# Kernel tuning notes

Measured on AMD Instinct MI355X. Metric: run time of the kernel, lower is better.

## Reference

```python
import jax, jax.numpy as jnp
import numpy as np

D = 768   # embedding_len
NL = 4    # nleft attributes
NR = 4    # nright attributes
LL = 256  # total left tokens
LR = 256  # total right tokens
DE = (NL + NR) * D  # entity-matching highway width


def setup_inputs() -> dict:
    key = jax.random.key(0)
    ks = jax.random.split(key, 12)
    f = lambda k, s: (jax.random.normal(k, s, jnp.float32) * 0.02)
    return {
        "left_emb": jax.random.normal(ks[0], (LL, D), jnp.float32),
        "right_emb": jax.random.normal(ks[1], (LR, D), jnp.float32),
        "Wn_tok": f(ks[2], (D, D)), "bn_tok": jnp.zeros((D,), jnp.float32),
        "Wg_tok": f(ks[3], (D, D)), "bg_tok": jnp.full((D,), -2.0, jnp.float32),
        "W_lin_tok": f(ks[4], (D, 1)), "b_lin_tok": jnp.zeros((1,), jnp.float32),
        "attr_emb_left": f(ks[5], (NL, D)),
        "attr_emb_right": f(ks[6], (NR, D)),
        "Wn_ent": f(ks[7], (DE, DE)), "bn_ent": jnp.zeros((DE,), jnp.float32),
        "Wg_ent": f(ks[8], (DE, DE)), "bg_ent": jnp.full((DE,), -2.0, jnp.float32),
        "W_lin_ent": f(ks[9], (DE, 2)), "b_lin_ent": jnp.zeros((2,), jnp.float32),
        "empty_attr_res": f(ks[10], (D,)),
        # per-attribute token counts; left includes an empty attribute
        "left_attrs_len": jnp.array([100, 80, 76, 0], dtype=jnp.int32),
        "right_attrs_len": jnp.array([64, 64, 64, 64], dtype=jnp.int32),
    }


def _highway(x, Wn, bn, Wg, bg):
    h = jax.nn.relu(x @ Wn + bn)
    g = jax.nn.sigmoid(x @ Wg + bg)
    return h * g + (1.0 - g) * x


def _token_matching(left, right, Wn, bn, Wg, bg, W_lin, b_lin):
    # compare_matrix: [L_left, L_right, D]
    cmp = jnp.abs(left[:, None, :] - right[None, :, :])
    hw = _highway(cmp, Wn, bn, Wg, bg)
    scores = hw @ W_lin + b_lin                     # [Ll, Lr, 1]
    # softmax over dim=1 (right tokens); only argmax is used downstream
    idx = jnp.argmax(scores[..., 0], axis=1)        # [Ll]
    return jnp.take_along_axis(cmp, idx[:, None, None], axis=1)[:, 0, :]  # [Ll, D]


def _attribute_matching(tokens, field_emb, cmp_res, lens, empty_attr):
    # ragged per-attribute softmax-weighted segment reduction
    n = field_emb.shape[0]
    L = tokens.shape[0]
    seg = jnp.repeat(jnp.arange(n), lens, total_repeat_length=L)   # [L]
    scores = jnp.einsum('ld,ld->l', tokens, field_emb[seg])        # [L]
    m = jax.ops.segment_max(scores, seg, num_segments=n)
    e = jnp.exp(scores - m[seg])
    z = jax.ops.segment_sum(e, seg, num_segments=n)
    w = e / z[seg]                                                  # softmax within segment
    reps = jax.ops.segment_sum(w[:, None] * cmp_res, seg, num_segments=n)  # [n, D]
    return jnp.where(lens[:, None] > 0, reps, empty_attr[None, :])


def reference(left_emb, right_emb, Wn_tok, bn_tok, Wg_tok, bg_tok,
              W_lin_tok, b_lin_tok, attr_emb_left, attr_emb_right,
              Wn_ent, bn_ent, Wg_ent, bg_ent, W_lin_ent, b_lin_ent,
              empty_attr_res, left_attrs_len, right_attrs_len):
    left_cmp = _token_matching(left_emb, right_emb, Wn_tok, bn_tok, Wg_tok, bg_tok,
                               W_lin_tok, b_lin_tok)
    right_cmp = _token_matching(right_emb, left_emb, Wn_tok, bn_tok, Wg_tok, bg_tok,
                                W_lin_tok, b_lin_tok)
    left_rep = _attribute_matching(left_emb, attr_emb_left, left_cmp,
                                   left_attrs_len, empty_attr_res)
    right_rep = _attribute_matching(right_emb, attr_emb_right, right_cmp,
                                    right_attrs_len, empty_attr_res)
    concat = jnp.concatenate([left_rep, right_rep], axis=0).reshape(1, -1)  # [1, DE]
    hw = _highway(concat, Wn_ent, bn_ent, Wg_ent, bg_ent)
    logits = hw @ W_lin_ent + b_lin_ent                                     # [1, 2]
    return jax.nn.softmax(logits, axis=1).flatten()                         # [2]
```

## Files before the change

### kernel.cpp

```cpp
#include <hip/hip_runtime.h>
#include <math.h>
#include <stdint.h>

#define DD 768
#define NT 256
#define DE 6144

typedef _Float16 half8 __attribute__((ext_vector_type(8)));
typedef _Float16 half4 __attribute__((ext_vector_type(4)));
typedef short short8 __attribute__((ext_vector_type(8)));
typedef float floatx4 __attribute__((ext_vector_type(4)));

__device__ __forceinline__ void async_ld16(const void* g, void* l) {
  __builtin_amdgcn_global_load_lds(
      (const __attribute__((address_space(1))) unsigned int*)g,
      (__attribute__((address_space(3))) unsigned int*)l, 16, 0, 0);
}

__global__ __launch_bounds__(256) void transpose_cvt(
    const float* __restrict__ Wn, const float* __restrict__ Wg,
    _Float16* __restrict__ WnT, _Float16* __restrict__ WgT)
{
  const float* W = blockIdx.z ? Wg : Wn;
  _Float16* WT = blockIdx.z ? WgT : WnT;
  __shared__ float tile[32][33];
  const int tx = threadIdx.x & 31, ty = threadIdx.x >> 5;
  const int d0 = blockIdx.x * 32, k0 = blockIdx.y * 32;
  #pragma unroll
  for (int p = 0; p < 4; ++p)
    tile[ty + p*8][tx] = W[(size_t)(k0 + ty + p*8)*DD + d0 + tx];
  __syncthreads();
  #pragma unroll
  for (int p = 0; p < 4; ++p) {
    const int d = d0 + ty + p*8;
    const int k = k0 + tx;
    const int idx = d*DD + (k & ~63) + ((((k >> 3) & 7) ^ (d & 7)) << 3) + (k & 7);
    WT[idx] = (_Float16)tile[tx][ty + p*8];
  }
}

__global__ __launch_bounds__(256) void cvt_lr(
    const float* __restrict__ L, const float* __restrict__ R,
    _Float16* __restrict__ Lh, _Float16* __restrict__ Rh)
{
  const float* src = blockIdx.y ? R : L;
  _Float16* dst = blockIdx.y ? Rh : Lh;
  const int o = blockIdx.x*1024 + threadIdx.x*4;
  float4 v = *(const float4*)&src[o];
  half4 h; h[0] = (_Float16)v.x; h[1] = (_Float16)v.y;
  h[2] = (_Float16)v.z; h[3] = (_Float16)v.w;
  *(half4*)&dst[o] = h;
}

__global__ __launch_bounds__(256, 2) void score_mfma(
    const _Float16* __restrict__ Lh, const _Float16* __restrict__ Rh,
    const _Float16* __restrict__ WnT, const _Float16* __restrict__ WgT,
    const float* __restrict__ bn, const float* __restrict__ bg,
    const float* __restrict__ Wl, float* __restrict__ Sp)
{
  const int jbase = blockIdx.x * 128;
  const int dbase = blockIdx.y * 128;
  const int i     = blockIdx.z;
  const int tid   = threadIdx.x;

  __shared__ _Float16 As [128*64];
  __shared__ _Float16 Bns[128*64];
  __shared__ _Float16 Bgs[128*64];

  floatx4 accn[4][4] = {};
  floatx4 accg[4][4] = {};

  const int kg = tid & 7;
  const int rl = tid >> 3;

  const int lane = tid & 63;
  const int wid  = tid >> 6;
  const int wj = (wid & 1) * 64;
  const int wd = (wid >> 1) * 64;
  const int m = lane & 15;
  const int q = lane >> 4;
  const int gq8 = ((q ^ (m & 7)) << 3);

  const int drow = lane >> 3;
  const int dseg = lane & 7;

  int aoff[4], boff[4];
  #pragma unroll
  for (int t4 = 0; t4 < 4; ++t4) {
    aoff[t4] = (wj + t4*16 + m) * 64;
    boff[t4] = (wd + t4*16 + m) * 64;
  }

  for (int k0 = 0; k0 < DD; k0 += 64) {
    #pragma unroll
    for (int t = 0; t < 4; ++t) {
      const int row = wid*32 + t*8 + drow;
      async_ld16(&WnT[(size_t)(dbase + row)*DD + k0 + dseg*8],
                 &Bns[(wid*32 + t*8)*64]);
      async_ld16(&WgT[(size_t)(dbase + row)*DD + k0 + dseg*8],
                 &Bgs[(wid*32 + t*8)*64]);
    }
    half8 l8 = *(const half8*)&Lh[i*DD + k0 + kg*8];
    #pragma unroll
    for (int rep = 0; rep < 4; ++rep) {
      const int row = rl + rep*32;
      half8 rv = *(const half8*)&Rh[(size_t)(jbase + row)*DD + k0 + kg*8];
      half8 dv8 = l8 - rv;
      short8 sb; __builtin_memcpy(&sb, &dv8, 16);
      sb &= (short)0x7FFF;
      *(short8*)&As[row*64 + ((kg ^ (row & 7)) << 3)] = sb;
    }
    __syncthreads();
    #pragma unroll
    for (int kk = 0; kk < 64; kk += 32) {
      const int ko = kk ^ gq8;
      half8 af[4], bfn[4], bfg[4];
      #pragma unroll
      for (int t4 = 0; t4 < 4; ++t4) af[t4] = *(const half8*)&As[aoff[t4] + ko];
      #pragma unroll
      for (int t4 = 0; t4 < 4; ++t4) {
        bfn[t4] = *(const half8*)&Bns[boff[t4] + ko];
        bfg[t4] = *(const half8*)&Bgs[boff[t4] + ko];
      }
      #pragma unroll
      for (int tj = 0; tj < 4; ++tj)
        #pragma unroll
        for (int td = 0; td < 4; ++td) {
          accn[tj][td] = __builtin_amdgcn_mfma_f32_16x16x32_f16(
              af[tj], bfn[td], accn[tj][td], 0, 0, 0);
          accg[tj][td] = __builtin_amdgcn_mfma_f32_16x16x32_f16(
              af[tj], bfg[td], accg[tj][td], 0, 0, 0);
        }
    }
    __syncthreads();
  }

  float bnv[4], bgv[4], wlv[4], lv[4];
  int dv[4];
  #pragma unroll
  for (int td = 0; td < 4; ++td) {
    const int d = dbase + wd + td*16 + m;
    dv[td] = d; bnv[td] = bn[d]; bgv[td] = bg[d]; wlv[td] = Wl[d];
    lv[td] = (float)Lh[i*DD + d];
  }
  const int jb = jbase + wj;
  const int plane = blockIdx.y * 2 + (wid >> 1);
  float* Sout = Sp + (size_t)plane * NT * NT + (size_t)i * NT;
  #pragma unroll
  for (int tj = 0; tj < 4; ++tj) {
    #pragma unroll
    for (int r = 0; r < 4; ++r) {
      const int j = jb + tj*16 + q*4 + r;
      float sc = 0.f;
      #pragma unroll
      for (int td = 0; td < 4; ++td) {
        const float nv = accn[tj][td][r] + bnv[td];
        const float gp = accg[tj][td][r] + bgv[td];
        const float g  = 1.f / (1.f + __expf(-gp));
        const float c  = fabsf(lv[td] - (float)Rh[(size_t)j*DD + dv[td]]);
        sc += (fmaxf(nv, 0.f)*g + (1.f - g)*c) * wlv[td];
      }
      sc += __shfl_xor(sc, 1, 16);
      sc += __shfl_xor(sc, 2, 16);
      sc += __shfl_xor(sc, 4, 16);
      sc += __shfl_xor(sc, 8, 16);
      if (m == 0) Sout[j] = sc;
    }
  }
}

__global__ __launch_bounds__(256) void argmax_attr(
    const float* __restrict__ Sp,
    int* __restrict__ idxL, int* __restrict__ idxR,
    const float* __restrict__ Lemb, const float* __restrict__ Remb,
    const float* __restrict__ AEl, const float* __restrict__ AEr,
    const int* __restrict__ lensL, const int* __restrict__ lensR,
    float* __restrict__ wS, int* __restrict__ segA)
{
  const int b = blockIdx.x;
  const int t = threadIdx.x;

  if (b < 2*NT) {
    const size_t off = (b < NT) ? ((size_t)b*NT + t) : ((size_t)t*NT + (b - NT));
    float v = 0.f;
    #pragma unroll
    for (int p = 0; p < 12; ++p) v += Sp[(size_t)p*NT*NT + off];
    int idx = t;
    #pragma unroll
    for (int mm = 1; mm < 64; mm <<= 1) {
      float ov = __shfl_xor(v, mm, 64);
      int   oi = __shfl_xor(idx, mm, 64);
      if (ov > v || (ov == v && oi < idx)) { v = ov; idx = oi; }
    }
    __shared__ float sv[4]; __shared__ int si[4];
    if ((t & 63) == 0) { sv[t>>6] = v; si[t>>6] = idx; }
    __syncthreads();
    if (t == 0) {
      #pragma unroll
      for (int w = 1; w < 4; ++w)
        if (sv[w] > v || (sv[w] == v && si[w] < idx)) { v = sv[w]; idx = si[w]; }
      if (b < NT) idxL[b] = idx; else idxR[b - NT] = idx;
    }
    return;
  }

  const int side = b - 2*NT;
  const float* tok = side ? Remb : Lemb;
  const float* AE  = side ? AEr  : AEl;
  const int* lens  = side ? lensR : lensL;
  const int c0 = lens[0], c1 = c0 + lens[1], c2 = c1 + lens[2];
  const int seg = (t < c0) ? 0 : (t < c1) ? 1 : (t < c2) ? 2 : 3;
  float s = 0.f;
  const float4* tr = (const float4*)&tok[(size_t)t*DD];
  const float4* ar = (const float4*)&AE[(size_t)seg*DD];
  for (int k = 0; k < DD/4; ++k) {
    float4 a = tr[k], bb = ar[k];
    s += a.x*bb.x + a.y*bb.y + a.z*bb.z + a.w*bb.w;
  }
  __shared__ float scS[NT]; __shared__ int segS[NT];
  __shared__ float mS[4], zS[4];
  scS[t] = s; segS[t] = seg;
  __syncthreads();
  if (t < 4) {
    float mx = -INFINITY;
    for (int u = 0; u < NT; ++u) if (segS[u] == t) mx = fmaxf(mx, scS[u]);
    mS[t] = mx;
    float z = 0.f;
    for (int u = 0; u < NT; ++u) if (segS[u] == t) z += __expf(scS[u] - mx);
    zS[t] = z;
  }
  __syncthreads();
  wS[side*NT + t] = __expf(s - mS[seg]) / zS[seg];
  segA[side*NT + t] = seg;
}

__global__ __launch_bounds__(256) void attr_reduce(
    const float* __restrict__ Lemb, const float* __restrict__ Remb,
    const int* __restrict__ lensL, const int* __restrict__ lensR,
    const int* __restrict__ idxL, const int* __restrict__ idxR,
    const float* __restrict__ wS, const int* __restrict__ segA,
    const float* __restrict__ empty, float* __restrict__ x)
{
  const int side = blockIdx.x;
  const float* tok = side ? Remb : Lemb;
  const float* oth = side ? Lemb : Remb;
  const int* lens  = side ? lensR : lensL;
  const int* idx   = side ? idxR  : idxL;
  const float* w   = wS + side*NT;
  const int* sg    = segA + side*NT;
  float* xo = x + side*4*DD;
  const int t = threadIdx.x;
  const int dl = t & 63, uq = t >> 6;
  const int d = blockIdx.y*64 + dl;
  float a0 = 0.f, a1 = 0.f, a2 = 0.f, a3 = 0.f;
  for (int u = uq*64; u < uq*64 + 64; ++u) {
    const float c = fabsf(tok[(size_t)u*DD + d] - oth[(size_t)idx[u]*DD + d]);
    const float wc = w[u] * c;
    const int s = sg[u];
    a0 += (s == 0) ? wc : 0.f;
    a1 += (s == 1) ? wc : 0.f;
    a2 += (s == 2) ? wc : 0.f;
    a3 += (s == 3) ? wc : 0.f;
  }
  __shared__ float red[4][4][64];
  red[uq][0][dl] = a0; red[uq][1][dl] = a1;
  red[uq][2][dl] = a2; red[uq][3][dl] = a3;
  __syncthreads();
  if (uq == 0) {
    #pragma unroll
    for (int s = 0; s < 4; ++s) {
      float v = red[0][s][dl] + red[1][s][dl] + red[2][s][dl] + red[3][s][dl];
      xo[s*DD + d] = (lens[s] > 0) ? v : empty[d];
    }
  }
}

__global__ __launch_bounds__(256) void ent_matvec4(
    const float* __restrict__ x,
    const float* __restrict__ Wn, const float* __restrict__ Wg,
    float* __restrict__ pn, float* __restrict__ pg)
{
  const float* W = blockIdx.z ? Wg : Wn;
  float* p = blockIdx.z ? pg : pn;
  __shared__ float xs[96];
  const int db = blockIdx.x;
  const int kb = blockIdx.y;
  const int tid = threadIdx.x;
  if (tid < 96) xs[tid] = x[kb*96 + tid];
  __syncthreads();
  const int col = db*1024 + tid*4;
  float4 a = {0.f,0.f,0.f,0.f};
  const size_t base = (size_t)kb*96*DE + col;
  #pragma unroll 8
  for (int kk = 0; kk < 96; ++kk) {
    const float xv = xs[kk];
    float4 w = *(const float4*)&W[base + (size_t)kk*DE];
    a.x = fmaf(xv, w.x, a.x); a.y = fmaf(xv, w.y, a.y);
    a.z = fmaf(xv, w.z, a.z); a.w = fmaf(xv, w.w, a.w);
  }
  *(float4*)&p[(size_t)kb*DE + col] = a;
}

__global__ __launch_bounds__(256) void ent_reduce(
    const float* __restrict__ pn, const float* __restrict__ pg,
    float* __restrict__ yn, float* __restrict__ yg)
{
  const int o = blockIdx.x*256 + threadIdx.x;
  float sn = 0.f, sg = 0.f;
  for (int kb = 0; kb < 64; ++kb) {
    sn += pn[(size_t)kb*DE + o];
    sg += pg[(size_t)kb*DE + o];
  }
  yn[o] = sn; yg[o] = sg;
}

__global__ __launch_bounds__(256) void final_kernel(
    const float* __restrict__ x, const float* __restrict__ yn,
    const float* __restrict__ yg, const float* __restrict__ bn,
    const float* __restrict__ bg, const float* __restrict__ Wl,
    const float* __restrict__ bl, float* __restrict__ out)
{
  const int tid = threadIdx.x;
  float a0 = 0.f, a1 = 0.f;
  for (int p = 0; p < DE/256; ++p) {
    int d = p*256 + tid;
    float n  = yn[d] + bn[d];
    float gp = yg[d] + bg[d];
    float h  = fmaxf(n, 0.f);
    float g  = 1.f / (1.f + __expf(-gp));
    float hw = h*g + (1.f - g)*x[d];
    a0 += hw * Wl[d*2 + 0];
    a1 += hw * Wl[d*2 + 1];
  }
  #pragma unroll
  for (int mm = 1; mm < 64; mm <<= 1) {
    a0 += __shfl_xor(a0, mm, 64);
    a1 += __shfl_xor(a1, mm, 64);
  }
  __shared__ float s0[4], s1[4];
  if ((tid & 63) == 0) { s0[tid>>6] = a0; s1[tid>>6] = a1; }
  __syncthreads();
  if (tid == 0) {
    for (int w = 1; w < 4; ++w) { a0 += s0[w]; a1 += s1[w]; }
    float l0 = a0 + bl[0], l1 = a1 + bl[1];
    float m = fmaxf(l0, l1);
    float e0 = __expf(l0 - m), e1 = __expf(l1 - m);
    out[0] = e0 / (e0 + e1);
    out[1] = e1 / (e0 + e1);
  }
}

extern "C" void kernel_launch(void* const* d_in, const int* in_sizes, int n_in,
                              void* d_out, int out_size, void* d_ws, size_t ws_size,
                              hipStream_t stream) {
  const float* Lemb   = (const float*)d_in[0];
  const float* Remb   = (const float*)d_in[1];
  const float* Wn_tok = (const float*)d_in[2];
  const float* bn_tok = (const float*)d_in[3];
  const float* Wg_tok = (const float*)d_in[4];
  const float* bg_tok = (const float*)d_in[5];
  const float* Wl_tok = (const float*)d_in[6];
  const float* AEl    = (const float*)d_in[8];
  const float* AEr    = (const float*)d_in[9];
  const float* Wn_ent = (const float*)d_in[10];
  const float* bn_ent = (const float*)d_in[11];
  const float* Wg_ent = (const float*)d_in[12];
  const float* bg_ent = (const float*)d_in[13];
  const float* Wl_ent = (const float*)d_in[14];
  const float* bl_ent = (const float*)d_in[15];
  const float* empty  = (const float*)d_in[16];
  const int*   lensL  = (const int*)d_in[17];
  const int*   lensR  = (const int*)d_in[18];

  char* ws = (char*)d_ws;
  float* Sp   = (float*)(ws + 0);
  float* pn   = (float*)(ws + 0);
  float* pg   = (float*)(ws + 1572864);
  int*  idxL  = (int*)  (ws + 3145728);
  int*  idxR  = (int*)  (ws + 3146752);
  float* x    = (float*)(ws + 3147776);
  float* yn   = (float*)(ws + 3172352);
  float* yg   = (float*)(ws + 3196928);
  float* wSm  = (float*)(ws + 3221504);
  int*  segA  = (int*)  (ws + 3223552);
  _Float16* WnT = (_Float16*)(ws + 3225600);
  _Float16* WgT = (_Float16*)(ws + 4405248);
  _Float16* Lh  = (_Float16*)(ws + 5584896);
  _Float16* Rh  = (_Float16*)(ws + 5978112);

  transpose_cvt<<<dim3(24, 24, 2), 256, 0, stream>>>(Wn_tok, Wg_tok, WnT, WgT);
  cvt_lr<<<dim3(192, 2), 256, 0, stream>>>(Lemb, Remb, Lh, Rh);
  score_mfma<<<dim3(2, 6, NT), 256, 0, stream>>>(
      Lh, Rh, WnT, WgT, bn_tok, bg_tok, Wl_tok, Sp);
  argmax_attr<<<514, 256, 0, stream>>>(
      Sp, idxL, idxR, Lemb, Remb, AEl, AEr, lensL, lensR, wSm, segA);
  attr_reduce<<<dim3(2, 12), 256, 0, stream>>>(
      Lemb, Remb, lensL, lensR, idxL, idxR, wSm, segA, empty, x);
  ent_matvec4<<<dim3(6, 64, 2), 256, 0, stream>>>(x, Wn_ent, Wg_ent, pn, pg);
  ent_reduce<<<24, 256, 0, stream>>>(pn, pg, yn, yg);
  final_kernel<<<1, 256, 0, stream>>>(
      x, yn, yg, bn_ent, bg_ent, Wl_ent, bl_ent, (float*)d_out);
}
```

Before: 649.8 us.

## Double-buffer LDS tiles in score_mfma to overlap loads with MFMA

After: 768.8 us. 1.18x slower.

```diff
diff --git a/kernel.cpp b/kernel.cpp
--- a/kernel.cpp
+++ b/kernel.cpp
@@ -63,9 +63,9 @@
   const int i     = blockIdx.z;
   const int tid   = threadIdx.x;
 
-  __shared__ _Float16 As [128*64];
-  __shared__ _Float16 Bns[128*64];
-  __shared__ _Float16 Bgs[128*64];
+  __shared__ _Float16 As [2][128*64];
+  __shared__ _Float16 Bns[2][128*64];
+  __shared__ _Float16 Bgs[2][128*64];
 
   floatx4 accn[4][4] = {};
   floatx4 accg[4][4] = {};
@@ -91,14 +91,14 @@
     boff[t4] = (wd + t4*16 + m) * 64;
   }
 
-  for (int k0 = 0; k0 < DD; k0 += 64) {
+  auto stage = [&](int k0, _Float16* As_, _Float16* Bns_, _Float16* Bgs_) {
     #pragma unroll
     for (int t = 0; t < 4; ++t) {
       const int row = wid*32 + t*8 + drow;
       async_ld16(&WnT[(size_t)(dbase + row)*DD + k0 + dseg*8],
-                 &Bns[(wid*32 + t*8)*64]);
+                 &Bns_[(wid*32 + t*8)*64]);
       async_ld16(&WgT[(size_t)(dbase + row)*DD + k0 + dseg*8],
-                 &Bgs[(wid*32 + t*8)*64]);
+                 &Bgs_[(wid*32 + t*8)*64]);
     }
     half8 l8 = *(const half8*)&Lh[i*DD + k0 + kg*8];
     #pragma unroll
@@ -108,19 +108,22 @@
       half8 dv8 = l8 - rv;
       short8 sb; __builtin_memcpy(&sb, &dv8, 16);
       sb &= (short)0x7FFF;
-      *(short8*)&As[row*64 + ((kg ^ (row & 7)) << 3)] = sb;
-    }
-    __syncthreads();
+      *(short8*)&As_[row*64 + ((kg ^ (row & 7)) << 3)] = sb;
+    }
+  };
+
+  auto compute = [&](const _Float16* As_, const _Float16* Bns_,
+                     const _Float16* Bgs_) {
     #pragma unroll
     for (int kk = 0; kk < 64; kk += 32) {
       const int ko = kk ^ gq8;
       half8 af[4], bfn[4], bfg[4];
       #pragma unroll
-      for (int t4 = 0; t4 < 4; ++t4) af[t4] = *(const half8*)&As[aoff[t4] + ko];
+      for (int t4 = 0; t4 < 4; ++t4) af[t4] = *(const half8*)&As_[aoff[t4] + ko];
       #pragma unroll
       for (int t4 = 0; t4 < 4; ++t4) {
-        bfn[t4] = *(const half8*)&Bns[boff[t4] + ko];
-        bfg[t4] = *(const half8*)&Bgs[boff[t4] + ko];
+        bfn[t4] = *(const half8*)&Bns_[boff[t4] + ko];
+        bfg[t4] = *(const half8*)&Bgs_[boff[t4] + ko];
       }
       #pragma unroll
       for (int tj = 0; tj < 4; ++tj)
@@ -132,6 +135,17 @@
               af[tj], bfg[td], accg[tj][td], 0, 0, 0);
         }
     }
+  };
+
+  stage(0, As[0], Bns[0], Bgs[0]);
+  __syncthreads();
+
+  for (int t = 0; t < 12; t += 2) {
+    stage((t + 1)*64, As[1], Bns[1], Bgs[1]);
+    compute(As[0], Bns[0], Bgs[0]);
+    __syncthreads();
+    if (t + 2 < 12) stage((t + 2)*64, As[0], Bns[0], Bgs[0]);
+    compute(As[1], Bns[1], Bgs[1]);
     __syncthreads();
   }
 
```

## Double-buffer score_mfma LDS tiles and widen blocks to cover all right tokens

Applied to the files above, without the earlier changes.

Result: slower. 669.6 us (+3.1%).

```diff
diff --git a/kernel.cpp b/kernel.cpp
--- a/kernel.cpp
+++ b/kernel.cpp
@@ -52,20 +52,19 @@
   *(half4*)&dst[o] = h;
 }
 
-__global__ __launch_bounds__(256, 2) void score_mfma(
+__global__ __launch_bounds__(512, 2) void score_mfma(
     const _Float16* __restrict__ Lh, const _Float16* __restrict__ Rh,
     const _Float16* __restrict__ WnT, const _Float16* __restrict__ WgT,
     const float* __restrict__ bn, const float* __restrict__ bg,
     const float* __restrict__ Wl, float* __restrict__ Sp)
 {
-  const int jbase = blockIdx.x * 128;
-  const int dbase = blockIdx.y * 128;
-  const int i     = blockIdx.z;
+  const int dbase = blockIdx.x * 128;
+  const int i     = blockIdx.y;
   const int tid   = threadIdx.x;
 
-  __shared__ _Float16 As [128*64];
-  __shared__ _Float16 Bns[128*64];
-  __shared__ _Float16 Bgs[128*64];
+  __shared__ _Float16 As [2][256*64];
+  __shared__ _Float16 Bns[2][128*64];
+  __shared__ _Float16 Bgs[2][128*64];
 
   floatx4 accn[4][4] = {};
   floatx4 accg[4][4] = {};
@@ -75,8 +74,8 @@
 
   const int lane = tid & 63;
   const int wid  = tid >> 6;
-  const int wj = (wid & 1) * 64;
-  const int wd = (wid >> 1) * 64;
+  const int wj = (wid & 3) * 64;
+  const int wd = (wid >> 2) * 64;
   const int m = lane & 15;
   const int q = lane >> 4;
   const int gq8 = ((q ^ (m & 7)) << 3);
@@ -84,55 +83,102 @@
   const int drow = lane >> 3;
   const int dseg = lane & 7;
 
-  int aoff[4], boff[4];
+  int arow[4], brow[4];
   #pragma unroll
   for (int t4 = 0; t4 < 4; ++t4) {
-    aoff[t4] = (wj + t4*16 + m) * 64;
-    boff[t4] = (wd + t4*16 + m) * 64;
-  }
-
-  for (int k0 = 0; k0 < DD; k0 += 64) {
-    #pragma unroll
-    for (int t = 0; t < 4; ++t) {
-      const int row = wid*32 + t*8 + drow;
-      async_ld16(&WnT[(size_t)(dbase + row)*DD + k0 + dseg*8],
-                 &Bns[(wid*32 + t*8)*64]);
-      async_ld16(&WgT[(size_t)(dbase + row)*DD + k0 + dseg*8],
-                 &Bgs[(wid*32 + t*8)*64]);
-    }
-    half8 l8 = *(const half8*)&Lh[i*DD + k0 + kg*8];
+    arow[t4] = (wj + t4*16 + m) * 64;
+    brow[t4] = (wd + t4*16 + m) * 64;
+  }
+
+  {
+    half8 l80 = *(const half8*)&Lh[i*DD + kg*8];
+    #pragma unroll
+    for (int tt = 0; tt < 2; ++tt) {
+      const int brow0 = wid*16 + tt*8;
+      async_ld16(&WnT[(size_t)(dbase + brow0 + drow)*DD + dseg*8],
+                 &Bns[0][brow0*64]);
+      async_ld16(&WgT[(size_t)(dbase + brow0 + drow)*DD + dseg*8],
+                 &Bgs[0][brow0*64]);
+    }
     #pragma unroll
     for (int rep = 0; rep < 4; ++rep) {
-      const int row = rl + rep*32;
-      half8 rv = *(const half8*)&Rh[(size_t)(jbase + row)*DD + k0 + kg*8];
-      half8 dv8 = l8 - rv;
+      const int row = rl + rep*64;
+      half8 rv = *(const half8*)&Rh[(size_t)row*DD + kg*8];
+      half8 dv8 = l80 - rv;
       short8 sb; __builtin_memcpy(&sb, &dv8, 16);
       sb &= (short)0x7FFF;
-      *(short8*)&As[row*64 + ((kg ^ (row & 7)) << 3)] = sb;
+      *(short8*)&As[0][row*64 + ((kg ^ (row & 7)) << 3)] = sb;
     }
     __syncthreads();
-    #pragma unroll
-    for (int kk = 0; kk < 64; kk += 32) {
-      const int ko = kk ^ gq8;
-      half8 af[4], bfn[4], bfg[4];
+  }
+
+  for (int t = 0; t < 12; ++t) {
+    const int c = t & 1;
+    const _Float16* Ac  = As [c];
+    const _Float16* Bnc = Bns[c];
+    const _Float16* Bgc = Bgs[c];
+    _Float16* An  = As [c ^ 1];
+    _Float16* Bnn = Bns[c ^ 1];
+    _Float16* Bgn = Bgs[c ^ 1];
+    const int k0n = (t + 1) * 64;
+    const bool st = (t < 11);
+
+    half8 l8n;
+    if (st) l8n = *(const half8*)&Lh[i*DD + k0n + kg*8];
+
+    #pragma unroll
+    for (int p = 0; p < 4; ++p) {
+      const int jh = p >> 1, dh = p & 1;
+      half8 af[2][2], bfn[2][2], bfg[2][2];
       #pragma unroll
-      for (int t4 = 0; t4 < 4; ++t4) af[t4] = *(const half8*)&As[aoff[t4] + ko];
+      for (int kki = 0; kki < 2; ++kki) {
+        const int ko = (kki*32) ^ gq8;
+        #pragma unroll
+        for (int u = 0; u < 2; ++u) {
+          af [kki][u] = *(const half8*)&Ac [arow[jh*2 + u] + ko];
+          bfn[kki][u] = *(const half8*)&Bnc[brow[dh*2 + u] + ko];
+          bfg[kki][u] = *(const half8*)&Bgc[brow[dh*2 + u] + ko];
+        }
+      }
+      half8 rv;
+      if (st) {
+        rv = *(const half8*)&Rh[(size_t)(rl + p*64)*DD + k0n + kg*8];
+        const int tt = p & 1;
+        const int brow0 = wid*16 + tt*8;
+        if (p < 2) {
+          async_ld16(&WnT[(size_t)(dbase + brow0 + drow)*DD + k0n + dseg*8],
+                     &Bnn[brow0*64]);
+        } else {
+          async_ld16(&WgT[(size_t)(dbase + brow0 + drow)*DD + k0n + dseg*8],
+                     &Bgn[brow0*64]);
+        }
+      }
+      __builtin_amdgcn_sched_barrier(0);
+      __builtin_amdgcn_s_barrier();
+      __builtin_amdgcn_sched_barrier(0);
+      __builtin_amdgcn_s_setprio(1);
       #pragma unroll
-      for (int t4 = 0; t4 < 4; ++t4) {
-        bfn[t4] = *(const half8*)&Bns[boff[t4] + ko];
-        bfg[t4] = *(const half8*)&Bgs[boff[t4] + ko];
+      for (int kki = 0; kki < 2; ++kki)
+        #pragma unroll
+        for (int u = 0; u < 2; ++u)
+          #pragma unroll
+          for (int v = 0; v < 2; ++v) {
+            accn[jh*2+u][dh*2+v] = __builtin_amdgcn_mfma_f32_16x16x32_f16(
+                af[kki][u], bfn[kki][v], accn[jh*2+u][dh*2+v], 0, 0, 0);
+            accg[jh*2+u][dh*2+v] = __builtin_amdgcn_mfma_f32_16x16x32_f16(
+                af[kki][u], bfg[kki][v], accg[jh*2+u][dh*2+v], 0, 0, 0);
+          }
+      __builtin_amdgcn_s_setprio(0);
+      if (st) {
+        const int row = rl + p*64;
+        half8 dv8 = l8n - rv;
+        short8 sb; __builtin_memcpy(&sb, &dv8, 16);
+        sb &= (short)0x7FFF;
+        *(short8*)&An[row*64 + ((kg ^ (row & 7)) << 3)] = sb;
       }
-      #pragma unroll
-      for (int tj = 0; tj < 4; ++tj)
-        #pragma unroll
-        for (int td = 0; td < 4; ++td) {
-          accn[tj][td] = __builtin_amdgcn_mfma_f32_16x16x32_f16(
-              af[tj], bfn[td], accn[tj][td], 0, 0, 0);
-          accg[tj][td] = __builtin_amdgcn_mfma_f32_16x16x32_f16(
-              af[tj], bfg[td], accg[tj][td], 0, 0, 0);
-        }
-    }
-    __syncthreads();
+      __builtin_amdgcn_sched_barrier(0);
+      __syncthreads();
+    }
   }
 
   float bnv[4], bgv[4], wlv[4], lv[4];
@@ -143,8 +189,8 @@
     dv[td] = d; bnv[td] = bn[d]; bgv[td] = bg[d]; wlv[td] = Wl[d];
     lv[td] = (float)Lh[i*DD + d];
   }
-  const int jb = jbase + wj;
-  const int plane = blockIdx.y * 2 + (wid >> 1);
+  const int jb = wj;
+  const int plane = blockIdx.x * 2 + (wid >> 2);
   float* Sout = Sp + (size_t)plane * NT * NT + (size_t)i * NT;
   #pragma unroll
   for (int tj = 0; tj < 4; ++tj) {
@@ -390,7 +436,7 @@
 
   transpose_cvt<<<dim3(24, 24, 2), 256, 0, stream>>>(Wn_tok, Wg_tok, WnT, WgT);
   cvt_lr<<<dim3(192, 2), 256, 0, stream>>>(Lemb, Remb, Lh, Rh);
-  score_mfma<<<dim3(2, 6, NT), 256, 0, stream>>>(
+  score_mfma<<<dim3(6, 256), 512, 0, stream>>>(
       Lh, Rh, WnT, WgT, bn_tok, bg_tok, Wl_tok, Sp);
   argmax_attr<<<514, 256, 0, stream>>>(
       Sp, idxL, idxR, Lemb, Remb, AEl, AEr, lensL, lensR, wSm, segA);
```
